# Optimization experiments

Measured on AMD Instinct MI355X. Metric: run time of the kernel, lower is better.

## Reference

```python
import jax, jax.numpy as jnp
import numpy as np

N_QUBITS = 4
N_LAYERS = 6
BATCH = 262144


def _apply_1q(state, U, wire):
    """Apply a 1-qubit gate U ((2,2) shared or (B,2,2) per-sample) on `wire`.
    state: (B, 2, 2, ..., 2) with n qubit axes after the batch axis."""
    s = jnp.moveaxis(state, 1 + wire, -1)
    shp = s.shape
    s2 = s.reshape(shp[0], -1, 2)
    if U.ndim == 3:
        s2 = jnp.einsum('bij,bkj->bki', U, s2)
    else:
        s2 = jnp.einsum('ij,bkj->bki', U, s2)
    return jnp.moveaxis(s2.reshape(shp), -1, 1 + wire)


def _apply_cnot(state, control, target):
    s = jnp.moveaxis(state, (1 + control, 1 + target), (-2, -1))
    shp = s.shape
    s2 = s.reshape(shp[0], -1, 2, 2)
    # flip target amplitudes where control bit is 1
    s2 = jnp.stack([s2[..., 0, :], s2[..., 1, ::-1]], axis=-2)
    return jnp.moveaxis(s2.reshape(shp), (-2, -1), (1 + control, 1 + target))


def _ry_batched(x):
    """RY(x) for x: (B,) -> (B,2,2) complex64 (real-valued matrix)."""
    c, s = jnp.cos(x / 2), jnp.sin(x / 2)
    m = jnp.stack([jnp.stack([c, -s], -1), jnp.stack([s, c], -1)], -2)
    return m.astype(jnp.complex64)


def _rot(phi, theta, omega):
    """qml.Rot = RZ(omega) RY(theta) RZ(phi), (2,2) complex64."""
    c, s = jnp.cos(theta / 2), jnp.sin(theta / 2)
    e = lambda a: jnp.exp(1j * a)
    m00 = e(-(phi + omega) / 2) * c
    m01 = -e((phi - omega) / 2) * s
    m10 = e(-(phi - omega) / 2) * s
    m11 = e((phi + omega) / 2) * c
    return jnp.stack([jnp.stack([m00, m01]), jnp.stack([m10, m11])]).astype(jnp.complex64)


def setup_inputs() -> dict:
    key = jax.random.key(0)
    k1, k2 = jax.random.split(key)
    inputs = jax.random.normal(k1, (BATCH, N_QUBITS), dtype=jnp.float32)
    quantum_weights = jax.random.uniform(k2, (N_LAYERS, N_QUBITS, 3), dtype=jnp.float32, minval=-0.05, maxval=0.05)
    return {"inputs": inputs, "quantum_weights": quantum_weights}


def reference(inputs, quantum_weights):
    B, n = inputs.shape
    L = quantum_weights.shape[0]
    # |0...0> state, batched
    state = jnp.zeros((B,) + (2,) * n, jnp.complex64)
    state = state.at[(slice(None),) + (0,) * n].set(1.0)
    # AngleEmbedding(rotation='Y'): RY(inputs[:, w]) on wire w
    for w in range(n):
        state = _apply_1q(state, _ry_batched(inputs[:, w]), w)
    # StronglyEntanglingLayers: Rot per wire, then ring of CNOTs with range r = l % (n-1) + 1
    for l in range(L):
        for w in range(n):
            state = _apply_1q(state, _rot(quantum_weights[l, w, 0], quantum_weights[l, w, 1], quantum_weights[l, w, 2]), w)
        r = l % (n - 1) + 1
        for w in range(n):
            state = _apply_cnot(state, w, (w + r) % n)
    # <Z_w> for each wire
    p = jnp.abs(state.reshape(B, -1)) ** 2  # (B, 2^n)
    bits = (jnp.arange(2 ** n)[:, None] >> jnp.arange(n - 1, -1, -1)[None, :]) & 1
    z = (1 - 2 * bits).astype(p.dtype)  # (2^n, n)
    return p @ z  # (B, n) float32
```

## Files before the change

### kernel.cpp

```cpp
#include <hip/hip_runtime.h>

#define N_QUBITS 4
#define N_LAYERS 6
#define NSTATES  16

__device__ __forceinline__ float2 cmul(float2 a, float2 b) {
    return make_float2(a.x * b.x - a.y * b.y, a.x * b.y + a.y * b.x);
}
__device__ __forceinline__ float2 cadd(float2 a, float2 b) {
    return make_float2(a.x + b.x, a.y + b.y);
}

__global__ void build_u_kernel(const float* __restrict__ weights,
                               float* __restrict__ U) {
    __shared__ float2 rotm[N_LAYERS][N_QUBITS][4];

    const int t = threadIdx.x;
    if (t < N_LAYERS * N_QUBITS) {
        const int l = t / N_QUBITS, w = t % N_QUBITS;
        const float phi   = weights[(l * N_QUBITS + w) * 3 + 0];
        const float theta = weights[(l * N_QUBITS + w) * 3 + 1];
        const float omega = weights[(l * N_QUBITS + w) * 3 + 2];
        float st, ct;
        sincosf(theta * 0.5f, &st, &ct);
        const float a1 = -(phi + omega) * 0.5f;
        const float a2 =  (phi - omega) * 0.5f;
        float s1, c1, s2, c2;
        sincosf(a1, &s1, &c1);
        sincosf(a2, &s2, &c2);
        rotm[l][w][0] = make_float2( c1 * ct,  s1 * ct);
        rotm[l][w][1] = make_float2(-c2 * st, -s2 * st);
        rotm[l][w][2] = make_float2( c2 * st, -s2 * st);
        rotm[l][w][3] = make_float2( c1 * ct, -s1 * ct);
    }
    __syncthreads();

    if (t < NSTATES) {
        float2 amp[NSTATES];
        #pragma unroll
        for (int i = 0; i < NSTATES; ++i)
            amp[i] = make_float2(i == t ? 1.0f : 0.0f, 0.0f);

        #pragma unroll
        for (int l = 0; l < N_LAYERS; ++l) {
            #pragma unroll
            for (int w = 0; w < N_QUBITS; ++w) {
                const int bit = 1 << (3 - w);
                const float2 m00 = rotm[l][w][0];
                const float2 m01 = rotm[l][w][1];
                const float2 m10 = rotm[l][w][2];
                const float2 m11 = rotm[l][w][3];
                #pragma unroll
                for (int i = 0; i < NSTATES; ++i) {
                    if (!(i & bit)) {
                        const int j = i | bit;
                        const float2 a0 = amp[i];
                        const float2 a1v = amp[j];
                        amp[i] = cadd(cmul(m00, a0), cmul(m01, a1v));
                        amp[j] = cadd(cmul(m10, a0), cmul(m11, a1v));
                    }
                }
            }
            const int r = l % (N_QUBITS - 1) + 1;
            #pragma unroll
            for (int w = 0; w < N_QUBITS; ++w) {
                const int cbit = 1 << (3 - w);
                const int tbit = 1 << (3 - ((w + r) % N_QUBITS));
                #pragma unroll
                for (int i = 0; i < NSTATES; ++i) {
                    if ((i & cbit) && !(i & tbit)) {
                        const int j = i | tbit;
                        const float2 tmp = amp[i];
                        amp[i] = amp[j];
                        amp[j] = tmp;
                    }
                }
            }
        }

        #pragma unroll
        for (int i = 0; i < NSTATES; ++i) {
            U[2 * (i * NSTATES + t) + 0] = amp[i].x;
            U[2 * (i * NSTATES + t) + 1] = amp[i].y;
        }
    }
}

__global__ __launch_bounds__(256) void qc_apply_kernel(
        const float* __restrict__ inputs,
        const float* __restrict__ U,
        float* __restrict__ out,
        int B) {
    const int b = blockIdx.x * blockDim.x + threadIdx.x;
    if (b >= B) return;

    const float4 xin = reinterpret_cast<const float4*>(inputs)[b];
    float s0, c0, s1, c1, s2, c2, s3, c3;
    __sincosf(xin.x * 0.5f, &s0, &c0);
    __sincosf(xin.y * 0.5f, &s1, &c1);
    __sincosf(xin.z * 0.5f, &s2, &c2);
    __sincosf(xin.w * 0.5f, &s3, &c3);

    float vA[4] = { c0 * c1, c0 * s1, s0 * c1, s0 * s1 };
    float vB[4] = { c2 * c3, c2 * s3, s2 * c3, s2 * s3 };
    float v[NSTATES];
    #pragma unroll
    for (int a = 0; a < 4; ++a)
        #pragma unroll
        for (int q = 0; q < 4; ++q)
            v[a * 4 + q] = vA[a] * vB[q];

    float p[NSTATES];
    #pragma unroll
    for (int i = 0; i < NSTATES; ++i) {
        float re = 0.0f, im = 0.0f;
        #pragma unroll
        for (int k = 0; k < NSTATES; ++k) {
            const float ur = U[2 * (i * NSTATES + k) + 0];
            const float ui = U[2 * (i * NSTATES + k) + 1];
            re = fmaf(ur, v[k], re);
            im = fmaf(ui, v[k], im);
        }
        p[i] = re * re + im * im;
    }

    float s0a[8], d0a[8];
    #pragma unroll
    for (int j = 0; j < 8; ++j) {
        s0a[j] = p[2 * j] + p[2 * j + 1];
        d0a[j] = p[2 * j] - p[2 * j + 1];
    }
    float z3 = ((d0a[0] + d0a[1]) + (d0a[2] + d0a[3])) +
               ((d0a[4] + d0a[5]) + (d0a[6] + d0a[7]));
    float s1a[4], d1a[4];
    #pragma unroll
    for (int j = 0; j < 4; ++j) {
        s1a[j] = s0a[2 * j] + s0a[2 * j + 1];
        d1a[j] = s0a[2 * j] - s0a[2 * j + 1];
    }
    float z2 = (d1a[0] + d1a[1]) + (d1a[2] + d1a[3]);
    float s2a0 = s1a[0] + s1a[1], s2a1 = s1a[2] + s1a[3];
    float d2a0 = s1a[0] - s1a[1], d2a1 = s1a[2] - s1a[3];
    float z1 = d2a0 + d2a1;
    float z0 = s2a0 - s2a1;

    reinterpret_cast<float4*>(out)[b] = make_float4(z0, z1, z2, z3);
}

extern "C" void kernel_launch(void* const* d_in, const int* in_sizes, int n_in,
                              void* d_out, int out_size, void* d_ws, size_t ws_size,
                              hipStream_t stream) {
    const float* inputs  = (const float*)d_in[0];
    const float* weights = (const float*)d_in[1];
    float* out = (float*)d_out;
    float* U   = (float*)d_ws;
    const int B = in_sizes[0] / N_QUBITS;

    build_u_kernel<<<1, 64, 0, stream>>>(weights, U);

    const int block = 256;
    const int grid = (B + block - 1) / block;
    qc_apply_kernel<<<grid, block, 0, stream>>>(inputs, U, out, B);
}
```

Baseline: 73.00 us.

## Parallelize unitary build across 256 threads and vectorize U row loads

The single-block kernel that builds the 16x16 circuit unitary now uses 256 threads, one per (column, amplitude) pair, holding the state in shared memory. Each gate is applied with a barrier between steps, and each layer's CNOT ring is folded into one index permutation, replacing 16 threads that each walked a fully unrolled register state serially. The apply kernel reads U rows as float4 instead of scalar loads. The build work is tiny, so the gain depends on how much that serial prologue cost against barrier overhead; the apply kernel's U loads were likely already uniform scalar loads.

```diff
diff --git a/kernel.cpp b/kernel.cpp
--- a/kernel.cpp
+++ b/kernel.cpp
@@ -11,79 +11,67 @@
     return make_float2(a.x + b.x, a.y + b.y);
 }
 
-__global__ void build_u_kernel(const float* __restrict__ weights,
-                               float* __restrict__ U) {
-    __shared__ float2 rotm[N_LAYERS][N_QUBITS][4];
+__global__ __launch_bounds__(256) void build_u_kernel(
+        const float* __restrict__ weights, float* __restrict__ U) {
+    __shared__ float2 rotm[N_LAYERS * N_QUBITS][4];
+    __shared__ float2 st[NSTATES][NSTATES];
 
     const int t = threadIdx.x;
     if (t < N_LAYERS * N_QUBITS) {
-        const int l = t / N_QUBITS, w = t % N_QUBITS;
-        const float phi   = weights[(l * N_QUBITS + w) * 3 + 0];
-        const float theta = weights[(l * N_QUBITS + w) * 3 + 1];
-        const float omega = weights[(l * N_QUBITS + w) * 3 + 2];
-        float st, ct;
-        sincosf(theta * 0.5f, &st, &ct);
+        const float phi   = weights[t * 3 + 0];
+        const float theta = weights[t * 3 + 1];
+        const float omega = weights[t * 3 + 2];
+        float stheta, ctheta;
+        sincosf(theta * 0.5f, &stheta, &ctheta);
         const float a1 = -(phi + omega) * 0.5f;
         const float a2 =  (phi - omega) * 0.5f;
         float s1, c1, s2, c2;
         sincosf(a1, &s1, &c1);
         sincosf(a2, &s2, &c2);
-        rotm[l][w][0] = make_float2( c1 * ct,  s1 * ct);
-        rotm[l][w][1] = make_float2(-c2 * st, -s2 * st);
-        rotm[l][w][2] = make_float2( c2 * st, -s2 * st);
-        rotm[l][w][3] = make_float2( c1 * ct, -s1 * ct);
+        rotm[t][0] = make_float2( c1 * ctheta,  s1 * ctheta);
+        rotm[t][1] = make_float2(-c2 * stheta, -s2 * stheta);
+        rotm[t][2] = make_float2( c2 * stheta, -s2 * stheta);
+        rotm[t][3] = make_float2( c1 * ctheta, -s1 * ctheta);
     }
+
+    const int c = t >> 4;
+    const int i = t & 15;
+    st[c][i] = make_float2(i == c ? 1.0f : 0.0f, 0.0f);
     __syncthreads();
 
-    if (t < NSTATES) {
-        float2 amp[NSTATES];
+    #pragma unroll 1
+    for (int l = 0; l < N_LAYERS; ++l) {
+        #pragma unroll 1
+        for (int w = 0; w < N_QUBITS; ++w) {
+            const int bit = 8 >> w;
+            if (!(i & bit)) {
+                const int j = i | bit;
+                const float2 a0 = st[c][i];
+                const float2 a1v = st[c][j];
+                const float2 m00 = rotm[l * N_QUBITS + w][0];
+                const float2 m01 = rotm[l * N_QUBITS + w][1];
+                const float2 m10 = rotm[l * N_QUBITS + w][2];
+                const float2 m11 = rotm[l * N_QUBITS + w][3];
+                st[c][i] = cadd(cmul(m00, a0), cmul(m01, a1v));
+                st[c][j] = cadd(cmul(m10, a0), cmul(m11, a1v));
+            }
+            __syncthreads();
+        }
+        const int r = l % (N_QUBITS - 1) + 1;
+        int fi = i;
         #pragma unroll
-        for (int i = 0; i < NSTATES; ++i)
-            amp[i] = make_float2(i == t ? 1.0f : 0.0f, 0.0f);
+        for (int w = 0; w < N_QUBITS; ++w) {
+            const int tb = 8 >> ((w + r) & 3);
+            if ((fi >> (3 - w)) & 1) fi ^= tb;
+        }
+        const float2 a = st[c][i];
+        __syncthreads();
+        st[c][fi] = a;
+        __syncthreads();
+    }
 
-        #pragma unroll
-        for (int l = 0; l < N_LAYERS; ++l) {
-            #pragma unroll
-            for (int w = 0; w < N_QUBITS; ++w) {
-                const int bit = 1 << (3 - w);
-                const float2 m00 = rotm[l][w][0];
-                const float2 m01 = rotm[l][w][1];
-                const float2 m10 = rotm[l][w][2];
-                const float2 m11 = rotm[l][w][3];
-                #pragma unroll
-                for (int i = 0; i < NSTATES; ++i) {
-                    if (!(i & bit)) {
-                        const int j = i | bit;
-                        const float2 a0 = amp[i];
-                        const float2 a1v = amp[j];
-                        amp[i] = cadd(cmul(m00, a0), cmul(m01, a1v));
-                        amp[j] = cadd(cmul(m10, a0), cmul(m11, a1v));
-                    }
-                }
-            }
-            const int r = l % (N_QUBITS - 1) + 1;
-            #pragma unroll
-            for (int w = 0; w < N_QUBITS; ++w) {
-                const int cbit = 1 << (3 - w);
-                const int tbit = 1 << (3 - ((w + r) % N_QUBITS));
-                #pragma unroll
-                for (int i = 0; i < NSTATES; ++i) {
-                    if ((i & cbit) && !(i & tbit)) {
-                        const int j = i | tbit;
-                        const float2 tmp = amp[i];
-                        amp[i] = amp[j];
-                        amp[j] = tmp;
-                    }
-                }
-            }
-        }
-
-        #pragma unroll
-        for (int i = 0; i < NSTATES; ++i) {
-            U[2 * (i * NSTATES + t) + 0] = amp[i].x;
-            U[2 * (i * NSTATES + t) + 1] = amp[i].y;
-        }
-    }
+    U[2 * (i * NSTATES + c) + 0] = st[c][i].x;
+    U[2 * (i * NSTATES + c) + 1] = st[c][i].y;
 }
 
 __global__ __launch_bounds__(256) void qc_apply_kernel(
@@ -101,8 +89,8 @@
     __sincosf(xin.z * 0.5f, &s2, &c2);
     __sincosf(xin.w * 0.5f, &s3, &c3);
 
-    float vA[4] = { c0 * c1, c0 * s1, s0 * c1, s0 * s1 };
-    float vB[4] = { c2 * c3, c2 * s3, s2 * c3, s2 * s3 };
+    const float vA[4] = { c0 * c1, c0 * s1, s0 * c1, s0 * s1 };
+    const float vB[4] = { c2 * c3, c2 * s3, s2 * c3, s2 * s3 };
     float v[NSTATES];
     #pragma unroll
     for (int a = 0; a < 4; ++a)
@@ -113,36 +101,36 @@
     float p[NSTATES];
     #pragma unroll
     for (int i = 0; i < NSTATES; ++i) {
+        const float4* row = reinterpret_cast<const float4*>(U + 2 * NSTATES * i);
         float re = 0.0f, im = 0.0f;
         #pragma unroll
-        for (int k = 0; k < NSTATES; ++k) {
-            const float ur = U[2 * (i * NSTATES + k) + 0];
-            const float ui = U[2 * (i * NSTATES + k) + 1];
-            re = fmaf(ur, v[k], re);
-            im = fmaf(ui, v[k], im);
+        for (int q = 0; q < 8; ++q) {
+            const float4 u4 = row[q];
+            re = fmaf(u4.x, v[2 * q],     re);
+            im = fmaf(u4.y, v[2 * q],     im);
+            re = fmaf(u4.z, v[2 * q + 1], re);
+            im = fmaf(u4.w, v[2 * q + 1], im);
         }
         p[i] = re * re + im * im;
     }
 
-    float s0a[8], d0a[8];
+    float sa[8], da[8];
     #pragma unroll
     for (int j = 0; j < 8; ++j) {
-        s0a[j] = p[2 * j] + p[2 * j + 1];
-        d0a[j] = p[2 * j] - p[2 * j + 1];
+        sa[j] = p[2 * j] + p[2 * j + 1];
+        da[j] = p[2 * j] - p[2 * j + 1];
     }
-    float z3 = ((d0a[0] + d0a[1]) + (d0a[2] + d0a[3])) +
-               ((d0a[4] + d0a[5]) + (d0a[6] + d0a[7]));
-    float s1a[4], d1a[4];
+    const float z3 = ((da[0] + da[1]) + (da[2] + da[3])) +
+                     ((da[4] + da[5]) + (da[6] + da[7]));
+    float sb[4], db[4];
     #pragma unroll
     for (int j = 0; j < 4; ++j) {
-        s1a[j] = s0a[2 * j] + s0a[2 * j + 1];
-        d1a[j] = s0a[2 * j] - s0a[2 * j + 1];
+        sb[j] = sa[2 * j] + sa[2 * j + 1];
+        db[j] = sa[2 * j] - sa[2 * j + 1];
     }
-    float z2 = (d1a[0] + d1a[1]) + (d1a[2] + d1a[3]);
-    float s2a0 = s1a[0] + s1a[1], s2a1 = s1a[2] + s1a[3];
-    float d2a0 = s1a[0] - s1a[1], d2a1 = s1a[2] - s1a[3];
-    float z1 = d2a0 + d2a1;
-    float z0 = s2a0 - s2a1;
+    const float z2 = (db[0] + db[1]) + (db[2] + db[3]);
+    const float z1 = (sb[0] - sb[1]) + (sb[2] - sb[3]);
+    const float z0 = (sb[0] + sb[1]) - (sb[2] + sb[3]);
 
     reinterpret_cast<float4*>(out)[b] = make_float4(z0, z1, z2, z3);
 }
@@ -156,7 +144,7 @@
     float* U   = (float*)d_ws;
     const int B = in_sizes[0] / N_QUBITS;
 
-    build_u_kernel<<<1, 64, 0, stream>>>(weights, U);
+    build_u_kernel<<<1, 256, 0, stream>>>(weights, U);
 
     const int block = 256;
     const int grid = (B + block - 1) / block;
```

Result: faster. 68.98 us (-5.5%).
